# Performance work log

Measured on AMD Instinct MI355X. Metric: run time of the kernel, lower is better.

Reference implementation:

```python
import jax, jax.numpy as jnp
import numpy as np

B, T, C = 2, 2048, 2048
H = 16          # n_head == n_kv_head
HD = 128        # head_size = hidden_dim // n_head (nope/value dim)
RD = 64         # qk_rope_head_dim
QLR = 1536      # q_lora_rank
KLR = 512       # kv_lora_rank
BASE = 10000.0
SCALE = (HD + RD) ** -0.5  # mscale = 1.0 since rope_scale = 1.0
EPS = 1e-6


def _rms(x, w):
    return x * jax.lax.rsqrt(jnp.mean(x * x, axis=-1, keepdims=True) + EPS) * w


def _rope_cos_sin(seq_len, dim):
    inv_freq = 1.0 / (BASE ** (jnp.arange(0, dim, 2, dtype=jnp.float32) / dim))
    t = jnp.arange(seq_len, dtype=jnp.float32)
    freqs = jnp.outer(t, inv_freq)            # [T, dim/2]
    emb = jnp.concatenate([freqs, freqs], -1)  # [T, dim]
    return jnp.cos(emb), jnp.sin(emb)


def _rotate_half(x):
    h = x.shape[-1] // 2
    return jnp.concatenate([-x[..., h:], x[..., :h]], axis=-1)


def setup_inputs() -> dict:
    key = jax.random.key(0)
    ks = jax.random.split(key, 8)
    s = 0.02
    return {
        "x": jax.random.normal(ks[0], (B, T, C), jnp.float32),
        "Wq_down": jax.random.normal(ks[1], (C, QLR), jnp.float32) * s,
        "q_norm_w": jnp.ones((QLR,), jnp.float32),
        "Wq_up": jax.random.normal(ks[2], (QLR, H * HD), jnp.float32) * s,
        "Wq_pe": jax.random.normal(ks[3], (QLR, H * RD), jnp.float32) * s,
        "Wkv_down": jax.random.normal(ks[4], (C, KLR), jnp.float32) * s,
        "kv_norm_w": jnp.ones((KLR,), jnp.float32),
        "Wkv_up": jax.random.normal(ks[5], (KLR, H * 2 * HD), jnp.float32) * s,
        "Wk_pe": jax.random.normal(ks[6], (C, RD), jnp.float32) * s,
        "k_pe_norm_w": jnp.ones((RD,), jnp.float32),
        "Wo": jax.random.normal(ks[7], (H * HD, C), jnp.float32) * s,
    }


def reference(x, Wq_down, q_norm_w, Wq_up, Wq_pe, Wkv_down, kv_norm_w,
              Wkv_up, Wk_pe, k_pe_norm_w, Wo):
    # ---- low-rank Q path ----
    cQ = _rms(x @ Wq_down, q_norm_w)                      # [B,T,QLR]
    q_nop = (cQ @ Wq_up).reshape(B, T, H, HD).transpose(0, 2, 1, 3)   # [B,H,T,HD]
    q_pe = (cQ @ Wq_pe).reshape(B, T, H, RD).transpose(0, 2, 1, 3)    # [B,H,T,RD]
    # ---- low-rank KV path ----
    cKV = _rms(x @ Wkv_down, kv_norm_w)                   # [B,T,KLR]
    kv = cKV @ Wkv_up                                     # [B,T,H*2*HD]
    k_nop, v = jnp.split(kv, 2, axis=-1)
    k_nop = k_nop.reshape(B, T, H, HD).transpose(0, 2, 1, 3)          # [B,H,T,HD]
    v = v.reshape(B, T, H, HD).transpose(0, 2, 1, 3)                  # [B,H,T,HD]
    # ---- decoupled RoPE key (shared across heads) ----
    k_pe = _rms(x @ Wk_pe, k_pe_norm_w).reshape(B, T, 1, RD).transpose(0, 2, 1, 3)  # [B,1,T,RD]
    cos, sin = _rope_cos_sin(T, RD)                       # [T,RD]
    q_pe = q_pe * cos + _rotate_half(q_pe) * sin
    k_pe = k_pe * cos + _rotate_half(k_pe) * sin
    # ---- concat nope + rope, causal SDPA ----
    q = jnp.concatenate([q_nop, q_pe], axis=-1)                           # [B,H,T,HD+RD]
    k = jnp.concatenate([k_nop, jnp.broadcast_to(k_pe, (B, H, T, RD))], axis=-1)
    scores = jnp.einsum('bhqd,bhkd->bhqk', q, k) * SCALE
    mask = jnp.tril(jnp.ones((T, T), dtype=bool))
    scores = jnp.where(mask, scores, jnp.finfo(scores.dtype).min)
    attn = jax.nn.softmax(scores, axis=-1)
    y = jnp.einsum('bhqk,bhkd->bhqd', attn, v)                            # [B,H,T,HD]
    y = y.transpose(0, 2, 1, 3).reshape(B, T, H * HD)
    return y @ Wo
```

## Files before the change

kernel.cpp:

```cpp
#include <hip/hip_runtime.h>
#include <hip/hip_bf16.h>
#include <cmath>

typedef __hip_bfloat16 bf16;
typedef __attribute__((ext_vector_type(8))) short s16x8;
typedef __attribute__((ext_vector_type(4))) float f32x4;

#define B_   2
#define T_   2048
#define C_   2048
#define H_   16
#define HD_  128
#define RD_  64
#define QLR_ 1536
#define KLR_ 512
#define SCALE_ 0.07216878364870322f

static __device__ __forceinline__ float b2f(bf16 v){ return __bfloat162float(v); }
static __device__ __forceinline__ bf16  f2b(float v){ return __float2bfloat16(v); }
static __device__ __forceinline__ float us2f(unsigned short u){
    union { unsigned short s[2]; float f; } v; v.s[0]=0; v.s[1]=u; return v.f;
}
static __device__ __forceinline__ float ldS(const void* p, size_t i, int isf32){
    return isf32 ? ((const float*)p)[i] : b2f(((const bf16*)p)[i]);
}
static __device__ __forceinline__ void ld4(const void* p, size_t i, int isf32, float* o){
    if (isf32) {
        float4 v = *(const float4*)((const float*)p + i);
        o[0]=v.x; o[1]=v.y; o[2]=v.z; o[3]=v.w;
    } else {
        ushort4 u = *(const ushort4*)((const bf16*)p + i);
        o[0]=us2f(u.x); o[1]=us2f(u.y); o[2]=us2f(u.z); o[3]=us2f(u.w);
    }
}

__global__ __launch_bounds__(64) void detect_kernel(const unsigned short* __restrict__ x,
                                                    int* __restrict__ flag)
{
    int big = 0;
    for (int i = threadIdx.x; i < 1024; i += 64) {
        const unsigned short u = x[2*i];
        const int e = (u >> 7) & 0xFF;
        if (e >= 139) big++;
    }
    #pragma unroll
    for (int off = 32; off; off >>= 1) big += __shfl_down(big, off, 64);
    if (threadIdx.x == 0) *flag = (big > 8) ? 1 : 0;
}

__global__ __launch_bounds__(256) void convert_kernel(const void* __restrict__ in,
                                                      bf16* __restrict__ out, int n,
                                                      const int* __restrict__ flag)
{
    const int f = *flag;
    const int i0 = (blockIdx.x * 256 + threadIdx.x) * 8;
    if (i0 >= n) return;
    float v[8];
    ld4(in, i0, f, v);
    ld4(in, i0 + 4, f, v + 4);
    bf16* o = out + i0;
    #pragma unroll
    for (int k = 0; k < 8; ++k) o[k] = f2b(v[k]);
}

struct TDesc { const void* in; bf16* out; int R, Cc, blkStart, nx; };
struct TBatch { TDesc d[5]; int nseg; };

__global__ __launch_bounds__(256) void transpose_batch(TBatch tb,
                                                       const int* __restrict__ flag)
{
    const int f = *flag;
    const int bid = blockIdx.x;
    int s = 0;
    #pragma unroll
    for (int i = 1; i < 5; ++i)
        if (i < tb.nseg && bid >= tb.d[i].blkStart) s = i;
    const TDesc d = tb.d[s];
    const int local = bid - d.blkStart;
    const int c0 = (local % d.nx) * 32;
    const int r0 = (local / d.nx) * 32;

    __shared__ float tile[32][33];
    const int tx = threadIdx.x & 31, ty = threadIdx.x >> 5;
    #pragma unroll
    for (int i = 0; i < 4; ++i)
        tile[ty + 8*i][tx] = ldS(d.in, (size_t)(r0 + ty + 8*i) * d.Cc + c0 + tx, f);
    __syncthreads();
    #pragma unroll
    for (int i = 0; i < 4; ++i)
        d.out[(size_t)(c0 + ty + 8*i) * d.R + r0 + tx] = f2b(tile[tx][ty + 8*i]);
}

__global__ __launch_bounds__(256) void transpose_v_kernel(const bf16* __restrict__ kvb,
                                                          bf16* __restrict__ vT)
{
    __shared__ bf16 tile[32][34];
    const int c0 = blockIdx.x * 32;
    const int r0 = blockIdx.y * 32;
    const int tx = threadIdx.x & 31, ty = threadIdx.x >> 5;
    #pragma unroll
    for (int i = 0; i < 4; ++i)
        tile[ty + 8*i][tx] = kvb[(size_t)(r0 + ty + 8*i) * (H_*256) + H_*128 + c0 + tx];
    __syncthreads();
    const int b  = r0 >> 11;
    const int t0 = r0 & (T_ - 1);
    #pragma unroll
    for (int i = 0; i < 4; ++i) {
        const int c  = c0 + ty + 8*i;
        const int hh = c >> 7, dd = c & 127;
        vT[(((size_t)b*H_ + hh)*HD_ + dd)*T_ + t0 + tx] = tile[tx][ty + 8*i];
    }
}

struct GOuts { void* p[3]; int start[3]; int stride[3]; int nseg; };

__global__ __launch_bounds__(256) void mfma_gemm(const bf16* __restrict__ A,
                                                 const bf16* __restrict__ BT,
                                                 GOuts go, int N, int K,
                                                 const int* __restrict__ flag, int cH)
{
    const int cf = cH ? *flag : 0;
    __shared__ bf16 As[128 * 32];
    __shared__ bf16 Bs[128 * 32];
    const int tid  = threadIdx.x;
    const int w    = tid >> 6;
    const int lane = tid & 63;
    const int quad = lane >> 4;
    const int l16  = lane & 15;
    const int wm   = w >> 1, wn = w & 1;
    const int bm   = blockIdx.y * 128, bn = blockIdx.x * 128;
    const int lrow = lane >> 2;
    const int lk   = (lane & 3) * 8;

    int seg = 0;
    #pragma unroll
    for (int i = 1; i < 3; ++i)
        if (i < go.nseg && bn >= go.start[i]) seg = i;
    void* const dstp   = go.p[seg];
    const int  dstoff  = go.start[seg];
    const int  dstride = go.stride[seg];

    f32x4 acc[4][4];
    #pragma unroll
    for (int i = 0; i < 4; ++i)
        #pragma unroll
        for (int j = 0; j < 4; ++j)
            acc[i][j] = (f32x4){0.f, 0.f, 0.f, 0.f};

    for (int kk = 0; kk < K; kk += 32) {
        if (kk) __syncthreads();
        #pragma unroll
        for (int c = 0; c < 2; ++c) {
            const int ch  = w * 2 + c;
            const int row = ch * 16 + lrow;
            const bf16* g = A + (size_t)(bm + row) * K + kk + lk;
            __builtin_amdgcn_global_load_lds(
                (const __attribute__((address_space(1))) unsigned int*)g,
                (__attribute__((address_space(3))) unsigned int*)(As + ch * 512),
                16, 0, 0);
        }
        #pragma unroll
        for (int c = 0; c < 2; ++c) {
            const int ch  = w * 2 + c;
            const int row = ch * 16 + lrow;
            const bf16* g = BT + (size_t)(bn + row) * K + kk + lk;
            __builtin_amdgcn_global_load_lds(
                (const __attribute__((address_space(1))) unsigned int*)g,
                (__attribute__((address_space(3))) unsigned int*)(Bs + ch * 512),
                16, 0, 0);
        }
        __syncthreads();

        s16x8 af[4], bfv[4];
        #pragma unroll
        for (int i = 0; i < 4; ++i)
            af[i] = *(const s16x8*)&As[(wm*64 + i*16 + l16) * 32 + quad*8];
        #pragma unroll
        for (int j = 0; j < 4; ++j)
            bfv[j] = *(const s16x8*)&Bs[(wn*64 + j*16 + l16) * 32 + quad*8];
        #pragma unroll
        for (int i = 0; i < 4; ++i)
            #pragma unroll
            for (int j = 0; j < 4; ++j)
                acc[i][j] = __builtin_amdgcn_mfma_f32_16x16x32_bf16(af[i], bfv[j], acc[i][j], 0, 0, 0);
    }

    #pragma unroll
    for (int i = 0; i < 4; ++i) {
        const int crow = bm + wm*64 + i*16 + quad*4;
        #pragma unroll
        for (int r = 0; r < 4; ++r) {
            #pragma unroll
            for (int j = 0; j < 4; ++j) {
                const int ccol = bn + wn*64 + j*16 + l16;
                if (ccol < N) {
                    const size_t idx = (size_t)(crow + r) * dstride + (ccol - dstoff);
                    if (cf) ((float*)dstp)[idx] = acc[i][j][r];
                    else    ((bf16*)dstp)[idx] = f2b(acc[i][j][r]);
                }
            }
        }
    }
}

template<int NPER>
__global__ __launch_bounds__(256) void rms_kernel(bf16* __restrict__ X,
                                                  const void* __restrict__ w,
                                                  const int* __restrict__ flag)
{
    const int wf = *flag;
    const int ncols = NPER * 256;
    __shared__ float red[4];
    const int row = blockIdx.x;
    const int tid = threadIdx.x;
    bf16* xr = X + (size_t)row * ncols;
    float vals[NPER];
    float ss = 0.f;
    #pragma unroll
    for (int i = 0; i < NPER; ++i) {
        float v = b2f(xr[tid + i*256]);
        vals[i] = v; ss += v*v;
    }
    #pragma unroll
    for (int off = 32; off; off >>= 1) ss += __shfl_down(ss, off, 64);
    if ((tid & 63) == 0) red[tid >> 6] = ss;
    __syncthreads();
    const float tot = red[0]+red[1]+red[2]+red[3];
    const float rs  = rsqrtf(tot / (float)ncols + 1e-6f);
    #pragma unroll
    for (int i = 0; i < NPER; ++i) {
        const int c = tid + i*256;
        xr[c] = f2b(vals[i] * rs * ldS(w, c, wf));
    }
}

__global__ __launch_bounds__(64) void kpe_rms_rope(bf16* __restrict__ X,
                                                   const void* __restrict__ w,
                                                   const int* __restrict__ flag)
{
    const int wf   = *flag;
    const int row  = blockIdx.x;
    const int t    = row & (T_ - 1);
    const int lane = threadIdx.x;
    bf16* xr = X + (size_t)row * RD_;
    const float v = b2f(xr[lane]);
    float ss = v * v;
    #pragma unroll
    for (int off = 32; off; off >>= 1) ss += __shfl_down(ss, off, 64);
    ss = __shfl(ss, 0, 64);
    const float rs = rsqrtf(ss / 64.f + 1e-6f);
    const float xn = v * rs * ldS(w, lane, wf);
    const int   i  = lane & 31;
    const float freq = powf(10000.f, -(float)(2*i) / 64.f);
    const float ang  = (float)t * freq;
    const float s = sinf(ang), c = cosf(ang);
    const float other = __shfl_xor(xn, 32, 64);
    const float o = (lane < 32) ? (xn * c - other * s) : (other * s + xn * c);
    xr[lane] = f2b(o);
}

__global__ __launch_bounds__(256) void qpe_rope(bf16* __restrict__ X)
{
    const int row = blockIdx.x;
    const int t   = row & (T_ - 1);
    bf16* xr = X + (size_t)row * (H_ * RD_);
    const int tid = threadIdx.x;
    #pragma unroll
    for (int pp = 0; pp < 2; ++pp) {
        const int p  = tid + pp * 256;
        const int hh = p >> 5;
        const int i  = p & 31;
        const int i0 = hh * 64 + i;
        const int i1 = i0 + 32;
        const float x1 = b2f(xr[i0]), x2 = b2f(xr[i1]);
        const float freq = powf(10000.f, -(float)(2*i) / 64.f);
        const float ang  = (float)t * freq;
        const float s = sinf(ang), c = cosf(ang);
        xr[i0] = f2b(x1 * c - x2 * s);
        xr[i1] = f2b(x1 * s + x2 * c);
    }
}

__global__ __launch_bounds__(256, 2) void flash_attn(const bf16* __restrict__ qnop,
                                                     const bf16* __restrict__ qpe,
                                                     const bf16* __restrict__ kv,
                                                     const bf16* __restrict__ kpe,
                                                     const bf16* __restrict__ vT,
                                                     bf16* __restrict__ y)
{
    __shared__ __align__(16) short Klds[64 * 192];
    __shared__ __align__(16) short Vt[128 * 64];
    __shared__ __align__(16) short Plds[4][16 * 64];

    const int h   = blockIdx.x;
    const int qt  = 31 - (int)blockIdx.y;
    const int b   = blockIdx.z;
    const int q0  = qt * 64;
    const int tid = threadIdx.x;
    const int w    = tid >> 6;
    const int lane = tid & 63;
    const int quad = lane >> 4;
    const int l16  = lane & 15;
    const int rk   = l16 & 7;
    const int rkp  = (l16 ^ (l16 >> 3)) & 7;
    const int row0 = q0 + w * 16;
    const size_t bT = (size_t)b * T_;
    const int bh  = b * H_ + h;

    const int kR = tid >> 4, kS = tid & 15;
    const int pR = tid >> 3, pS = tid & 7;
    const int vD = tid >> 3, vS = tid & 7;

    const bf16* gK = kv  + (bT + kR) * (H_*256) + h*128 + kS*8;
    const bf16* gP = kpe + (bT + pR) * RD_ + pS*8;
    const bf16* gV = vT  + ((size_t)bh*HD_ + vD) * T_ + vS*8;

    short* const wK = &Klds[kR*192 + ((kS ^ (kR & 7)) << 3)];
    short* const wP = &Klds[pR*192 + 128 + ((pS ^ (pR & 7)) << 3)];
    short* const wV = &Vt[vD*64 + ((vS ^ (vD & 7)) << 3)];

    s16x8 aq[6];
    {
        const size_t r = bT + row0 + l16;
        const bf16* qn = qnop + r * (H_*128) + h*128 + quad*8;
        #pragma unroll
        for (int kk = 0; kk < 4; ++kk) aq[kk] = *(const s16x8*)(qn + kk*32);
        const bf16* qp = qpe + r * (H_*64) + h*64 + quad*8;
        aq[4] = *(const s16x8*)(qp);
        aq[5] = *(const s16x8*)(qp + 32);
    }

    f32x4 o[8];
    #pragma unroll
    for (int i = 0; i < 8; ++i) o[i] = (f32x4){0.f,0.f,0.f,0.f};
    float m_run[4] = {-1e30f,-1e30f,-1e30f,-1e30f};
    float l_run[4] = {0.f,0.f,0.f,0.f};

    uint4 k0, k1, k2, k3, p0, p1, v0, v1, v2, v3;
    #define PF(J0) do {                                                     \
        const bf16* a_ = gK + (size_t)(J0) * (H_*256);                      \
        k0 = *(const uint4*)(a_);                                           \
        k1 = *(const uint4*)(a_ + 16*(H_*256));                             \
        k2 = *(const uint4*)(a_ + 32*(H_*256));                             \
        k3 = *(const uint4*)(a_ + 48*(H_*256));                             \
        const bf16* p_ = gP + (size_t)(J0) * RD_;                           \
        p0 = *(const uint4*)(p_);                                           \
        p1 = *(const uint4*)(p_ + 32*RD_);                                  \
        const bf16* v_ = gV + (J0);                                         \
        v0 = *(const uint4*)(v_);                                           \
        v1 = *(const uint4*)(v_ + 32*T_);                                   \
        v2 = *(const uint4*)(v_ + 64*T_);                                   \
        v3 = *(const uint4*)(v_ + 96*T_);                                   \
    } while (0)

    PF(0);

    const int ntiles = qt + 1;
    for (int it = 0; it < ntiles; ++it) {
        const int j0 = it * 64;
        asm volatile("s_waitcnt lgkmcnt(0)\n\ts_barrier" ::: "memory");

        *(uint4*)(wK)          = k0;
        *(uint4*)(wK + 16*192) = k1;
        *(uint4*)(wK + 32*192) = k2;
        *(uint4*)(wK + 48*192) = k3;
        *(uint4*)(wP)          = p0;
        *(uint4*)(wP + 32*192) = p1;
        *(uint4*)(wV)          = v0;
        *(uint4*)(wV + 32*64)  = v1;
        *(uint4*)(wV + 64*64)  = v2;
        *(uint4*)(wV + 96*64)  = v3;

        if (it + 1 < ntiles) PF(j0 + 64);

        asm volatile("s_waitcnt lgkmcnt(0)\n\ts_barrier" ::: "memory");

        if (j0 <= row0 + 15) {
            const bool needmask = (j0 + 63 > row0);
            f32x4 s[4];
            #pragma unroll
            for (int nsub = 0; nsub < 4; ++nsub) {
                f32x4 acc = (f32x4){0.f,0.f,0.f,0.f};
                #pragma unroll
                for (int kk = 0; kk < 6; ++kk) {
                    const s16x8 bk = *(const s16x8*)&Klds[(nsub*16 + l16)*192
                                        + ((((kk << 2) | quad) ^ rk) << 3)];
                    acc = __builtin_amdgcn_mfma_f32_16x16x32_bf16(aq[kk], bk, acc, 0, 0, 0);
                }
                #pragma unroll
                for (int reg = 0; reg < 4; ++reg) acc[reg] *= SCALE_;
                s[nsub] = acc;
            }
            if (needmask) {
                #pragma unroll
                for (int nsub = 0; nsub < 4; ++nsub)
                    #pragma unroll
                    for (int reg = 0; reg < 4; ++reg) {
                        const int col = j0 + nsub*16 + l16;
                        const int row = row0 + quad*4 + reg;
                        if (col > row) s[nsub][reg] = -1e30f;
                    }
            }
            float mt[4], alpha[4], rs[4];
            #pragma unroll
            for (int reg = 0; reg < 4; ++reg)
                mt[reg] = fmaxf(fmaxf(s[0][reg], s[1][reg]), fmaxf(s[2][reg], s[3][reg]));
            #pragma unroll
            for (int d = 1; d < 16; d <<= 1)
                #pragma unroll
                for (int reg = 0; reg < 4; ++reg)
                    mt[reg] = fmaxf(mt[reg], __shfl_xor(mt[reg], d, 64));
            #pragma unroll
            for (int reg = 0; reg < 4; ++reg) {
                const float mnew = fmaxf(m_run[reg], mt[reg]);
                alpha[reg] = __expf(m_run[reg] - mnew);
                m_run[reg] = mnew;
                rs[reg] = 0.f;
            }
            #pragma unroll
            for (int nsub = 0; nsub < 4; ++nsub)
                #pragma unroll
                for (int reg = 0; reg < 4; ++reg) {
                    const float p = __expf(s[nsub][reg] - m_run[reg]);
                    s[nsub][reg] = p;
                    rs[reg] += p;
                }
            #pragma unroll
            for (int d = 1; d < 16; d <<= 1)
                #pragma unroll
                for (int reg = 0; reg < 4; ++reg)
                    rs[reg] += __shfl_xor(rs[reg], d, 64);
            #pragma unroll
            for (int reg = 0; reg < 4; ++reg)
                l_run[reg] = l_run[reg] * alpha[reg] + rs[reg];

            #pragma unroll
            for (int nsub = 0; nsub < 4; ++nsub)
                #pragma unroll
                for (int reg = 0; reg < 4; ++reg) {
                    const bf16 pv = f2b(s[nsub][reg]);
                    const int prow = (quad << 2) + reg;
                    const int pk   = (prow ^ (prow >> 3)) & 7;
                    const int pby  = ((nsub << 5) + (l16 << 1)) ^ (pk << 4);
                    Plds[w][prow*64 + (pby >> 1)] = *(const short*)&pv;
                }
            #pragma unroll
            for (int n2 = 0; n2 < 8; ++n2)
                #pragma unroll
                for (int reg = 0; reg < 4; ++reg)
                    o[n2][reg] *= alpha[reg];

            const s16x8 ap0 = *(const s16x8*)&Plds[w][l16*64 + (((quad    ) ^ rkp) << 3)];
            const s16x8 ap1 = *(const s16x8*)&Plds[w][l16*64 + (((quad | 4) ^ rkp) << 3)];
            #pragma unroll
            for (int n2 = 0; n2 < 8; ++n2) {
                const s16x8 bv0 = *(const s16x8*)&Vt[(n2*16 + l16)*64 + (((quad    ) ^ rk) << 3)];
                const s16x8 bv1 = *(const s16x8*)&Vt[(n2*16 + l16)*64 + (((quad | 4) ^ rk) << 3)];
                o[n2] = __builtin_amdgcn_mfma_f32_16x16x32_bf16(ap0, bv0, o[n2], 0, 0, 0);
                o[n2] = __builtin_amdgcn_mfma_f32_16x16x32_bf16(ap1, bv1, o[n2], 0, 0, 0);
            }
        }
    }
    #undef PF

    #pragma unroll
    for (int reg = 0; reg < 4; ++reg) {
        const float inv = 1.f / l_run[reg];
        const size_t r = bT + row0 + quad*4 + reg;
        bf16* yr = y + r * (H_*128) + h*128 + l16;
        #pragma unroll
        for (int n2 = 0; n2 < 8; ++n2)
            yr[n2*16] = f2b(o[n2][reg] * inv);
    }
}

extern "C" void kernel_launch(void* const* d_in, const int* in_sizes, int n_in,
                              void* d_out, int out_size, void* d_ws, size_t ws_size,
                              hipStream_t stream)
{
    const void* x         = d_in[0];
    const void* Wq_down   = d_in[1];
    const void* q_norm_w  = d_in[2];
    const void* Wq_up     = d_in[3];
    const void* Wq_pe     = d_in[4];
    const void* Wkv_down  = d_in[5];
    const void* kv_norm_w = d_in[6];
    const void* Wkv_up    = d_in[7];
    const void* Wk_pe     = d_in[8];
    const void* kpe_nw    = d_in[9];
    const void* Wo        = d_in[10];

    char* ws = (char*)d_ws;
    int*  flag = (int*)(ws + 0);
    bf16* xb   = (bf16*)(ws + 256);
    bf16* cQ   = (bf16*)(ws + 16777472);
    bf16* cKV  = (bf16*)(ws + 29360384);
    bf16* kpeb = (bf16*)(ws + 33554688);
    bf16* qnop = (bf16*)(ws + 34078976);
    bf16* qpeb = (bf16*)(ws + 50856192);
    bf16* kvb  = (bf16*)(ws + 59244800);
    bf16* yb   = (bf16*)(ws + 92799232);

    bf16* P1 = kvb;
    bf16* P2 = (bf16*)((char*)kvb + 8912896);
    bf16* P3 = cQ;
    bf16* P4 = (bf16*)((char*)cQ + 4194304);
    bf16* vT = xb;

    const dim3 blk(256);

    detect_kernel<<<1, dim3(64), 0, stream>>>((const unsigned short*)x, flag);
    convert_kernel<<<(B_*T_*C_)/(256*8), blk, 0, stream>>>(x, xb, B_*T_*C_, flag);

    {
        TBatch tb;
        tb.d[0] = { Wq_down,  P1,               C_,  QLR_,     0, QLR_/32 };
        tb.d[1] = { Wkv_down, P1 + 1536*2048,   C_,  KLR_,  3072, KLR_/32 };
        tb.d[2] = { Wk_pe,    P1 + 2048*2048,   C_,  RD_,   4096, RD_/32  };
        tb.d[3] = { Wq_up,    P2,               QLR_, 2048, 4224, 2048/32 };
        tb.d[4] = { Wq_pe,    P2 + 2048*1536,   QLR_, 1024, 7296, 1024/32 };
        tb.nseg = 5;
        transpose_batch<<<8832, blk, 0, stream>>>(tb, flag);
    }

    {
        GOuts go; go.nseg = 3;
        go.p[0]=cQ;   go.start[0]=0;    go.stride[0]=QLR_;
        go.p[1]=cKV;  go.start[1]=1536; go.stride[1]=KLR_;
        go.p[2]=kpeb; go.start[2]=2048; go.stride[2]=RD_;
        mfma_gemm<<<dim3(17, 32), blk, 0, stream>>>(xb, P1, go, 2112, C_, flag, 0);
    }
    rms_kernel<6><<<B_*T_, blk, 0, stream>>>(cQ, q_norm_w, flag);
    rms_kernel<2><<<B_*T_, blk, 0, stream>>>(cKV, kv_norm_w, flag);
    kpe_rms_rope<<<B_*T_, dim3(64), 0, stream>>>(kpeb, kpe_nw, flag);

    {
        GOuts go; go.nseg = 2;
        go.p[0]=qnop; go.start[0]=0;    go.stride[0]=H_*HD_;
        go.p[1]=qpeb; go.start[1]=2048; go.stride[1]=H_*RD_;
        go.p[2]=nullptr; go.start[2]=0; go.stride[2]=0;
        mfma_gemm<<<dim3(24, 32), blk, 0, stream>>>(cQ, P2, go, 3072, QLR_, flag, 0);
    }
    qpe_rope<<<B_*T_, blk, 0, stream>>>(qpeb);

    {
        TBatch tb;
        tb.d[0] = { Wkv_up, P3, KLR_, H_*2*HD_,    0, (H_*2*HD_)/32 };
        tb.d[1] = { Wo,     P4, H_*HD_, C_,     2048, C_/32 };
        tb.d[2] = tb.d[1]; tb.d[3] = tb.d[1]; tb.d[4] = tb.d[1];
        tb.nseg = 2;
        transpose_batch<<<6144, blk, 0, stream>>>(tb, flag);
    }

    {
        GOuts go; go.nseg = 1;
        go.p[0]=kvb; go.start[0]=0; go.stride[0]=H_*2*HD_;
        go.p[1]=nullptr; go.start[1]=0; go.stride[1]=0;
        go.p[2]=nullptr; go.start[2]=0; go.stride[2]=0;
        mfma_gemm<<<dim3(32, 32), blk, 0, stream>>>(cKV, P3, go, H_*2*HD_, KLR_, flag, 0);
    }
    transpose_v_kernel<<<dim3((H_*HD_)/32, (B_*T_)/32), blk, 0, stream>>>(kvb, vT);

    flash_attn<<<dim3(H_, T_/64, B_), blk, 0, stream>>>(qnop, qpeb, kvb, kpeb, vT, yb);

    {
        GOuts go; go.nseg = 1;
        go.p[0]=d_out; go.start[0]=0; go.stride[0]=C_;
        go.p[1]=nullptr; go.start[1]=0; go.stride[1]=0;
        go.p[2]=nullptr; go.start[2]=0; go.stride[2]=0;
        mfma_gemm<<<dim3(C_/128, 32), blk, 0, stream>>>(yb, P4, go, C_, H_*HD_, flag, 1);
    }
}
```

Before: 490.4 us.

## Replace 128-tile GEMMs with 256x256 double-buffered direct-to-LDS MFMA kernel

Adds a 512-thread GEMM with 256x256 output tiles, K-steps of 64, double-buffered LDS filled with global_load_lds, swizzled LDS reads and s_setprio around the MFMA bursts. All four projection GEMMs use it. The k_pe column slice, which is not a multiple of 256, is split off into a separate small launch of the old kernel through a new column-offset argument. The goal is more data reuse per tile and overlap of global loads with MFMA work. The cost is 128KB of dynamic LDS per block and fewer blocks in flight, with no bounds checks, so it relies on dimensions that divide evenly.

```diff
diff --git a/kernel.cpp b/kernel.cpp
--- a/kernel.cpp
+++ b/kernel.cpp
@@ -117,7 +117,8 @@
 __global__ __launch_bounds__(256) void mfma_gemm(const bf16* __restrict__ A,
                                                  const bf16* __restrict__ BT,
                                                  GOuts go, int N, int K,
-                                                 const int* __restrict__ flag, int cH)
+                                                 const int* __restrict__ flag, int cH,
+                                                 int bnOff)
 {
     const int cf = cH ? *flag : 0;
     __shared__ bf16 As[128 * 32];
@@ -128,7 +129,7 @@
     const int quad = lane >> 4;
     const int l16  = lane & 15;
     const int wm   = w >> 1, wn = w & 1;
-    const int bm   = blockIdx.y * 128, bn = blockIdx.x * 128;
+    const int bm   = blockIdx.y * 128, bn = (blockIdx.x + bnOff) * 128;
     const int lrow = lane >> 2;
     const int lk   = (lane & 3) * 8;
 
@@ -198,6 +199,146 @@
                     if (cf) ((float*)dstp)[idx] = acc[i][j][r];
                     else    ((bf16*)dstp)[idx] = f2b(acc[i][j][r]);
                 }
+            }
+        }
+    }
+}
+
+__global__ __launch_bounds__(512, 2) void gemm256(const bf16* __restrict__ A,
+                                                  const bf16* __restrict__ BT,
+                                                  GOuts go, int N, int K,
+                                                  const int* __restrict__ flag, int cH)
+{
+    extern __shared__ __align__(16) char smem[];
+    const int cf   = cH ? *flag : 0;
+    const int tid  = threadIdx.x;
+    const int lane = tid & 63;
+    const int quad = lane >> 4;
+    const int l16  = lane & 15;
+    const int wid  = tid >> 6;
+    const int wm   = wid >> 2, wn = wid & 3;
+    const int bm   = blockIdx.y * 256, bn = blockIdx.x * 256;
+
+    int seg = 0;
+    #pragma unroll
+    for (int i = 1; i < 3; ++i)
+        if (i < go.nseg && bn >= go.start[i]) seg = i;
+    void* const dstp   = go.p[seg];
+    const int  dstoff  = go.start[seg];
+    const int  dstride = go.stride[seg];
+
+    const int nkt = K >> 6;
+    const int nit = nkt >> 1;
+
+    const int sl   = lane ^ (((lane >> 5) & 1) << 1);
+    const int sCol = (sl & 7) * 8;
+    const int sR   = tid >> 3;
+    const int s2   = ((l16 >> 2) & 1) << 1;
+    const int cq   = quad ^ s2;
+    const int aBase = wm*16384 + l16*128 + cq*16;
+    const int bBase = 32768 + (wn>>1)*16384 + ((wn&1)*64 + l16)*128 + cq*16;
+
+    f32x4 acc[8][4];
+    #pragma unroll
+    for (int i = 0; i < 8; ++i)
+        #pragma unroll
+        for (int j = 0; j < 4; ++j)
+            acc[i][j] = (f32x4){0.f,0.f,0.f,0.f};
+
+    s16x8 ar[4][2];
+    s16x8 br[2][2][2];
+
+    #define STG(op, buf, half, kt) do {                                          \
+        const int ktc_ = ((kt) < nkt ? (kt) : nkt-1);                            \
+        const bf16* base_ = (op) ? BT : A;                                       \
+        const int rb_ = ((op) ? bn : bm) + (half)*128;                           \
+        char* ld_ = smem + (buf)*65536 + (op)*32768 + (half)*16384;              \
+        _Pragma("unroll")                                                        \
+        for (int j_ = 0; j_ < 2; ++j_) {                                         \
+            const bf16* g_ = base_ + (size_t)(rb_ + j_*64 + sR) * K              \
+                             + ktc_*64 + sCol;                                   \
+            __builtin_amdgcn_global_load_lds(                                    \
+                (const __attribute__((address_space(1))) unsigned int*)g_,       \
+                (__attribute__((address_space(3))) unsigned int*)(ld_ + j_*8192 + tid*16), \
+                16, 0, 0);                                                       \
+        }                                                                        \
+    } while (0)
+
+    #define LDA(buf, qm) do {                                                    \
+        _Pragma("unroll")                                                        \
+        for (int mm_ = 0; mm_ < 4; ++mm_)                                        \
+            _Pragma("unroll")                                                    \
+            for (int ks_ = 0; ks_ < 2; ++ks_)                                    \
+                ar[mm_][ks_] = *(const s16x8*)(smem + (buf)*65536 + aBase        \
+                                               + ((qm)*4+mm_)*2048 + ks_*64);    \
+    } while (0)
+
+    #define LDB(buf, qn) do {                                                    \
+        _Pragma("unroll")                                                        \
+        for (int nn_ = 0; nn_ < 2; ++nn_)                                        \
+            _Pragma("unroll")                                                    \
+            for (int ks_ = 0; ks_ < 2; ++ks_)                                    \
+                br[qn][nn_][ks_] = *(const s16x8*)(smem + (buf)*65536 + bBase    \
+                                               + ((qn)*2+nn_)*2048 + ks_*64);    \
+    } while (0)
+
+    #define MM(qm, qn) do {                                                      \
+        __builtin_amdgcn_s_setprio(1);                                           \
+        _Pragma("unroll")                                                        \
+        for (int mm_ = 0; mm_ < 4; ++mm_)                                        \
+            _Pragma("unroll")                                                    \
+            for (int nn_ = 0; nn_ < 2; ++nn_)                                    \
+                _Pragma("unroll")                                                \
+                for (int ks_ = 0; ks_ < 2; ++ks_)                                \
+                    acc[(qm)*4+mm_][(qn)*2+nn_] =                                \
+                        __builtin_amdgcn_mfma_f32_16x16x32_bf16(                 \
+                            ar[mm_][ks_], br[qn][nn_][ks_],                      \
+                            acc[(qm)*4+mm_][(qn)*2+nn_], 0, 0, 0);               \
+        __builtin_amdgcn_s_setprio(0);                                           \
+    } while (0)
+
+    #define BARR __builtin_amdgcn_s_barrier()
+    #define VMC(n) asm volatile("s_waitcnt vmcnt(" #n ")" ::: "memory")
+
+    STG(0,0,0, 0); STG(0,0,1, 0); STG(1,0,0, 0); STG(1,0,1, 0);
+    STG(0,1,0, 1);
+    VMC(0); BARR;
+
+    for (int i = 0; i < nit; ++i) {
+        const int tB = 2*i + 1;
+        const int tA = 2*i + 2;
+        const int tC = 2*i + 3;
+
+        LDA(0,0); LDB(0,0); STG(0,1,1, tB); BARR; MM(0,0); BARR;
+        LDB(0,1);           STG(1,1,0, tB); BARR; MM(0,1); BARR;
+        LDA(0,1);           STG(1,1,1, tB); BARR; MM(1,1); BARR;
+        STG(0,0,0, tA); VMC(2); BARR; MM(1,0); BARR;
+        LDA(1,0); LDB(1,0); STG(0,0,1, tA); BARR; MM(0,0); BARR;
+        LDB(1,1);           STG(1,0,0, tA); BARR; MM(0,1); BARR;
+        LDA(1,1);           STG(1,0,1, tA); BARR; MM(1,1); BARR;
+        STG(0,1,0, tC); VMC(2); BARR; MM(1,0); BARR;
+    }
+
+    VMC(0);
+
+    #undef STG
+    #undef LDA
+    #undef LDB
+    #undef MM
+    #undef BARR
+    #undef VMC
+
+    #pragma unroll
+    for (int mm = 0; mm < 8; ++mm) {
+        const int crow = bm + wm*128 + mm*16 + quad*4;
+        #pragma unroll
+        for (int r = 0; r < 4; ++r) {
+            #pragma unroll
+            for (int nn = 0; nn < 4; ++nn) {
+                const int ccol = bn + wn*64 + nn*16 + l16;
+                const size_t idx = (size_t)(crow + r) * dstride + (ccol - dstoff);
+                if (cf) ((float*)dstp)[idx] = acc[mm][nn][r];
+                else    ((bf16*)dstp)[idx] = f2b(acc[mm][nn][r]);
             }
         }
     }
@@ -508,6 +649,14 @@
     bf16* vT = xb;
 
     const dim3 blk(256);
+    const dim3 blk512(512);
+
+    static int attr_set = 0;
+    if (!attr_set) {
+        hipFuncSetAttribute(reinterpret_cast<const void*>(gemm256),
+                            hipFuncAttributeMaxDynamicSharedMemorySize, 131072);
+        attr_set = 1;
+    }
 
     detect_kernel<<<1, dim3(64), 0, stream>>>((const unsigned short*)x, flag);
     convert_kernel<<<(B_*T_*C_)/(256*8), blk, 0, stream>>>(x, xb, B_*T_*C_, flag);
@@ -524,11 +673,18 @@
     }
 
     {
-        GOuts go; go.nseg = 3;
+        GOuts go; go.nseg = 2;
         go.p[0]=cQ;   go.start[0]=0;    go.stride[0]=QLR_;
         go.p[1]=cKV;  go.start[1]=1536; go.stride[1]=KLR_;
-        go.p[2]=kpeb; go.start[2]=2048; go.stride[2]=RD_;
-        mfma_gemm<<<dim3(17, 32), blk, 0, stream>>>(xb, P1, go, 2112, C_, flag, 0);
+        go.p[2]=nullptr; go.start[2]=0; go.stride[2]=0;
+        gemm256<<<dim3(8, 16), blk512, 131072, stream>>>(xb, P1, go, 2048, C_, flag, 0);
+    }
+    {
+        GOuts go; go.nseg = 1;
+        go.p[0]=kpeb; go.start[0]=2048; go.stride[0]=RD_;
+        go.p[1]=nullptr; go.start[1]=0; go.stride[1]=0;
+        go.p[2]=nullptr; go.start[2]=0; go.stride[2]=0;
+        mfma_gemm<<<dim3(1, 32), blk, 0, stream>>>(xb, P1, go, 2112, C_, flag, 0, 16);
     }
     rms_kernel<6><<<B_*T_, blk, 0, stream>>>(cQ, q_norm_w, flag);
     rms_kernel<2><<<B_*T_, blk, 0, stream>>>(cKV, kv_norm_w, flag);
@@ -539,7 +695,7 @@
         go.p[0]=qnop; go.start[0]=0;    go.stride[0]=H_*HD_;
         go.p[1]=qpeb; go.start[1]=2048; go.stride[1]=H_*RD_;
         go.p[2]=nullptr; go.start[2]=0; go.stride[2]=0;
-        mfma_gemm<<<dim3(24, 32), blk, 0, stream>>>(cQ, P2, go, 3072, QLR_, flag, 0);
+        gemm256<<<dim3(12, 16), blk512, 131072, stream>>>(cQ, P2, go, 3072, QLR_, flag, 0);
     }
     qpe_rope<<<B_*T_, blk, 0, stream>>>(qpeb);
 
@@ -557,7 +713,7 @@
         go.p[0]=kvb; go.start[0]=0; go.stride[0]=H_*2*HD_;
         go.p[1]=nullptr; go.start[1]=0; go.stride[1]=0;
         go.p[2]=nullptr; go.start[2]=0; go.stride[2]=0;
-        mfma_gemm<<<dim3(32, 32), blk, 0, stream>>>(cKV, P3, go, H_*2*HD_, KLR_, flag, 0);
+        gemm256<<<dim3(16, 16), blk512, 131072, stream>>>(cKV, P3, go, H_*2*HD_, KLR_, flag, 0);
     }
     transpose_v_kernel<<<dim3((H_*HD_)/32, (B_*T_)/32), blk, 0, stream>>>(kvb, vT);
 
@@ -568,6 +724,6 @@
         go.p[0]=d_out; go.start[0]=0; go.stride[0]=C_;
         go.p[1]=nullptr; go.start[1]=0; go.stride[1]=0;
         go.p[2]=nullptr; go.start[2]=0; go.stride[2]=0;
-        mfma_gemm<<<dim3(C_/128, 32), blk, 0, stream>>>(yb, P4, go, C_, H_*HD_, flag, 1);
-    }
-}
+        gemm256<<<dim3(8, 16), blk512, 131072, stream>>>(yb, P4, go, C_, H_*HD_, flag, 1);
+    }
+}
```

Result: slower. 539.6 us (+10.0%).

## Double-buffer MFMA GEMM with BK=64 and XOR-swizzled LDS tiles

Applied to the files above, without the earlier changes.

The bf16 MFMA GEMM now uses two 32 KB LDS buffers and a K-tile of 64. The next tile's global-to-LDS loads are issued before the current tile's fragment reads and MFMAs, so memory traffic overlaps compute and there is one barrier per tile. The LDS layout is XOR-swizzled by row to avoid bank conflicts on the fragment reads. MFMA issue is wrapped in s_setprio, and launch bounds request 2 blocks per CU. The cost is 64 KB of LDS per block and an unrolled loop that assumes an even number of K tiles.

```diff
diff --git a/kernel.cpp b/kernel.cpp
--- a/kernel.cpp
+++ b/kernel.cpp
@@ -114,23 +114,20 @@
 
 struct GOuts { void* p[3]; int start[3]; int stride[3]; int nseg; };
 
-__global__ __launch_bounds__(256) void mfma_gemm(const bf16* __restrict__ A,
-                                                 const bf16* __restrict__ BT,
-                                                 GOuts go, int N, int K,
-                                                 const int* __restrict__ flag, int cH)
-{
-    const int cf = cH ? *flag : 0;
-    __shared__ bf16 As[128 * 32];
-    __shared__ bf16 Bs[128 * 32];
+__global__ __launch_bounds__(256, 2) void mfma_gemm(const bf16* __restrict__ A,
+                                                    const bf16* __restrict__ BT,
+                                                    GOuts go, int N, int K,
+                                                    const int* __restrict__ flag, int cH)
+{
+    __shared__ __align__(16) char smem[65536];
+    const int cf   = cH ? *flag : 0;
     const int tid  = threadIdx.x;
-    const int w    = tid >> 6;
     const int lane = tid & 63;
     const int quad = lane >> 4;
     const int l16  = lane & 15;
+    const int w    = tid >> 6;
     const int wm   = w >> 1, wn = w & 1;
     const int bm   = blockIdx.y * 128, bn = blockIdx.x * 128;
-    const int lrow = lane >> 2;
-    const int lk   = (lane & 3) * 8;
 
     int seg = 0;
     #pragma unroll
@@ -140,6 +137,16 @@
     const int  dstoff  = go.start[seg];
     const int  dstride = go.stride[seg];
 
+    const int nkt = K >> 6;
+
+    const int sR   = tid >> 3;
+    const int sCol = ((tid & 7) ^ (sR & 7)) * 8;
+    const bf16* gA = A  + (size_t)(bm + sR) * K + sCol;
+    const bf16* gB = BT + (size_t)(bn + sR) * K + sCol;
+    const int rxk  = l16 & 7;
+    const int aOff = (wm*64 + l16) * 128;
+    const int bOff = 16384 + (wn*64 + l16) * 128;
+
     f32x4 acc[4][4];
     #pragma unroll
     for (int i = 0; i < 4; ++i)
@@ -147,43 +154,75 @@
         for (int j = 0; j < 4; ++j)
             acc[i][j] = (f32x4){0.f, 0.f, 0.f, 0.f};
 
-    for (int kk = 0; kk < K; kk += 32) {
-        if (kk) __syncthreads();
-        #pragma unroll
-        for (int c = 0; c < 2; ++c) {
-            const int ch  = w * 2 + c;
-            const int row = ch * 16 + lrow;
-            const bf16* g = A + (size_t)(bm + row) * K + kk + lk;
-            __builtin_amdgcn_global_load_lds(
-                (const __attribute__((address_space(1))) unsigned int*)g,
-                (__attribute__((address_space(3))) unsigned int*)(As + ch * 512),
-                16, 0, 0);
-        }
-        #pragma unroll
-        for (int c = 0; c < 2; ++c) {
-            const int ch  = w * 2 + c;
-            const int row = ch * 16 + lrow;
-            const bf16* g = BT + (size_t)(bn + row) * K + kk + lk;
-            __builtin_amdgcn_global_load_lds(
-                (const __attribute__((address_space(1))) unsigned int*)g,
-                (__attribute__((address_space(3))) unsigned int*)(Bs + ch * 512),
-                16, 0, 0);
-        }
-        __syncthreads();
-
-        s16x8 af[4], bfv[4];
-        #pragma unroll
-        for (int i = 0; i < 4; ++i)
-            af[i] = *(const s16x8*)&As[(wm*64 + i*16 + l16) * 32 + quad*8];
-        #pragma unroll
-        for (int j = 0; j < 4; ++j)
-            bfv[j] = *(const s16x8*)&Bs[(wn*64 + j*16 + l16) * 32 + quad*8];
-        #pragma unroll
-        for (int i = 0; i < 4; ++i)
-            #pragma unroll
-            for (int j = 0; j < 4; ++j)
-                acc[i][j] = __builtin_amdgcn_mfma_f32_16x16x32_bf16(af[i], bfv[j], acc[i][j], 0, 0, 0);
-    }
+    s16x8 af[4][2], bf[4][2];
+
+    #define STG(buf, kt) do {                                                    \
+        const int ke_ = ((kt) < nkt ? (kt) : nkt-1) * 64;                        \
+        _Pragma("unroll")                                                        \
+        for (int j_ = 0; j_ < 4; ++j_)                                           \
+            __builtin_amdgcn_global_load_lds(                                    \
+                (const __attribute__((address_space(1))) unsigned int*)          \
+                    (gA + (size_t)(j_*32) * K + ke_),                            \
+                (__attribute__((address_space(3))) unsigned int*)                \
+                    (smem + (buf)*32768 + j_*4096 + tid*16), 16, 0, 0);          \
+        _Pragma("unroll")                                                        \
+        for (int j_ = 0; j_ < 4; ++j_)                                           \
+            __builtin_amdgcn_global_load_lds(                                    \
+                (const __attribute__((address_space(1))) unsigned int*)          \
+                    (gB + (size_t)(j_*32) * K + ke_),                            \
+                (__attribute__((address_space(3))) unsigned int*)                \
+                    (smem + (buf)*32768 + 16384 + j_*4096 + tid*16), 16, 0, 0);  \
+    } while (0)
+
+    #define LD(buf) do {                                                         \
+        _Pragma("unroll")                                                        \
+        for (int i_ = 0; i_ < 4; ++i_)                                           \
+            _Pragma("unroll")                                                    \
+            for (int ks_ = 0; ks_ < 2; ++ks_)                                    \
+                af[i_][ks_] = *(const s16x8*)(smem + (buf)*32768 + aOff          \
+                              + i_*2048 + ((((ks_<<2)|quad) ^ rxk) << 4));       \
+        _Pragma("unroll")                                                        \
+        for (int j_ = 0; j_ < 4; ++j_)                                           \
+            _Pragma("unroll")                                                    \
+            for (int ks_ = 0; ks_ < 2; ++ks_)                                    \
+                bf[j_][ks_] = *(const s16x8*)(smem + (buf)*32768 + bOff          \
+                              + j_*2048 + ((((ks_<<2)|quad) ^ rxk) << 4));       \
+    } while (0)
+
+    #define MM do {                                                              \
+        __builtin_amdgcn_s_setprio(1);                                           \
+        _Pragma("unroll")                                                        \
+        for (int i_ = 0; i_ < 4; ++i_)                                           \
+            _Pragma("unroll")                                                    \
+            for (int j_ = 0; j_ < 4; ++j_)                                       \
+                _Pragma("unroll")                                                \
+                for (int ks_ = 0; ks_ < 2; ++ks_)                                \
+                    acc[i_][j_] = __builtin_amdgcn_mfma_f32_16x16x32_bf16(       \
+                        af[i_][ks_], bf[j_][ks_], acc[i_][j_], 0, 0, 0);         \
+        __builtin_amdgcn_s_setprio(0);                                           \
+    } while (0)
+
+    #define DRAIN asm volatile("s_waitcnt vmcnt(0)" ::: "memory");               \
+                  __builtin_amdgcn_s_barrier()
+
+    STG(0, 0);
+    DRAIN;
+
+    for (int t = 0; t < nkt; t += 2) {
+        STG(1, t+1);
+        LD(0);
+        MM;
+        DRAIN;
+        STG(0, t+2);
+        LD(1);
+        MM;
+        DRAIN;
+    }
+
+    #undef STG
+    #undef LD
+    #undef MM
+    #undef DRAIN
 
     #pragma unroll
     for (int i = 0; i < 4; ++i) {
```

Measured after the change: 455.7 us. -7.1%, faster.
